# Kernel tuning notes

Hardware: AMD Instinct MI355X
Metric: run time of the kernel (lower is better)

## Reference

```python
import jax, jax.numpy as jnp
import numpy as np

B, S, D, H, L, V = 8, 512, 1024, 16, 12, 30145
FF = 4 * D
NL = 2  # n_langs
EPS = 1e-12


def _ln(x, g, b):
    m = jnp.mean(x, axis=-1, keepdims=True)
    v = jnp.var(x, axis=-1, keepdims=True)
    return (x - m) * jax.lax.rsqrt(v + EPS) * g + b


def setup_inputs() -> dict:
    key = jax.random.key(0)
    ks = iter(jax.random.split(key, 32))
    std, estd = 0.02, 0.02
    d = {
        "input_ids": jax.random.randint(next(ks), (B, S), 0, V),
        "langs": jax.random.randint(next(ks), (B, S), 0, NL),
        "attention_mask": jnp.ones((B, S), jnp.float32),
        "word_emb": jax.random.normal(next(ks), (V, D), jnp.float32) * estd,
        "pos_emb": jax.random.normal(next(ks), (S, D), jnp.float32) * estd,
        "lang_emb": jax.random.normal(next(ks), (NL, D), jnp.float32) * estd,
        "ln_emb_g": jnp.ones((D,), jnp.float32),
        "ln_emb_b": jnp.zeros((D,), jnp.float32),
        "Wq": jax.random.normal(next(ks), (L, D, D), jnp.float32) * std,
        "bq": jnp.zeros((L, D), jnp.float32),
        "Wk": jax.random.normal(next(ks), (L, D, D), jnp.float32) * std,
        "bk": jnp.zeros((L, D), jnp.float32),
        "Wv": jax.random.normal(next(ks), (L, D, D), jnp.float32) * std,
        "bv": jnp.zeros((L, D), jnp.float32),
        "Wo": jax.random.normal(next(ks), (L, D, D), jnp.float32) * std,
        "bo": jnp.zeros((L, D), jnp.float32),
        "ln1_g": jnp.ones((L, D), jnp.float32),
        "ln1_b": jnp.zeros((L, D), jnp.float32),
        "W1": jax.random.normal(next(ks), (L, D, FF), jnp.float32) * std,
        "b1": jnp.zeros((L, FF), jnp.float32),
        "W2": jax.random.normal(next(ks), (L, FF, D), jnp.float32) * std,
        "b2": jnp.zeros((L, D), jnp.float32),
        "ln2_g": jnp.ones((L, D), jnp.float32),
        "ln2_b": jnp.zeros((L, D), jnp.float32),
    }
    return d


def reference(input_ids, langs, attention_mask, word_emb, pos_emb, lang_emb,
              ln_emb_g, ln_emb_b, Wq, bq, Wk, bk, Wv, bv, Wo, bo,
              ln1_g, ln1_b, W1, b1, W2, b2, ln2_g, ln2_b):
    dh = D // H
    scale = 1.0 / np.sqrt(dh).astype(np.float32)
    # embeddings: word + position + language, then LayerNorm, then pad-mask
    x = word_emb[input_ids] + pos_emb[None, :, :] + lang_emb[langs]  # [B,S,D]
    x = _ln(x, ln_emb_g, ln_emb_b)
    fmask = attention_mask  # [B,S], 1=keep
    x = x * fmask[:, :, None]
    neg = (-1e30) * (1.0 - fmask)[:, None, None, :]  # [B,1,1,S] additive mask

    def layer(x, p):
        Wq_, bq_, Wk_, bk_, Wv_, bv_, Wo_, bo_, g1, gb1, W1_, b1_, W2_, b2_, g2, gb2 = p
        q = ((x @ Wq_ + bq_) * scale).reshape(B, S, H, dh)
        k = (x @ Wk_ + bk_).reshape(B, S, H, dh)
        v = (x @ Wv_ + bv_).reshape(B, S, H, dh)
        scores = jnp.einsum('bqhd,bkhd->bhqk', q, k) + neg
        w = jax.nn.softmax(scores, axis=-1)
        ctx = jnp.einsum('bhqk,bkhd->bqhd', w, v).reshape(B, S, D)
        x = _ln(x + ctx @ Wo_ + bo_, g1, gb1)
        h = jax.nn.gelu(x @ W1_ + b1_, approximate=False)  # erf gelu as in source
        x = _ln(x + h @ W2_ + b2_, g2, gb2)
        x = x * fmask[:, :, None]
        return x, None

    params = (Wq, bq, Wk, bk, Wv, bv, Wo, bo, ln1_g, ln1_b, W1, b1, W2, b2, ln2_g, ln2_b)
    x, _ = jax.lax.scan(layer, x, params)
    return x
```

## Files before the change

### kernel.cpp

```cpp
#include <hip/hip_runtime.h>
#include <math.h>

typedef float  f32x4  __attribute__((ext_vector_type(4)));
typedef __bf16 bf16x8 __attribute__((ext_vector_type(8)));
typedef __bf16 bf16x4 __attribute__((ext_vector_type(4)));

#define DEV __device__ __forceinline__

DEV f32x4 mfma16(bf16x8 a, bf16x8 b, f32x4 c) {
    return __builtin_amdgcn_mfma_f32_16x16x32_bf16(a, b, c, 0, 0, 0);
}

DEV void async16(const void* g, void* l) {
    __builtin_amdgcn_global_load_lds((const __attribute__((address_space(1))) void*)g,
                                     (__attribute__((address_space(3))) void*)l, 16, 0, 0);
}

constexpr int B_  = 8;
constexpr int S_  = 512;
constexpr int D_  = 1024;
constexpr int H_  = 16;
constexpr int FF_ = 4096;
constexpr int ROWS = B_ * S_;

__global__ __launch_bounds__(256)
void embed_ln_kernel(const int* __restrict__ ids, const int* __restrict__ lgs,
                     const float* __restrict__ fmask,
                     const float* __restrict__ wemb, const float* __restrict__ pemb,
                     const float* __restrict__ lemb,
                     const float* __restrict__ g, const float* __restrict__ bb,
                     __bf16* __restrict__ xb)
{
    __shared__ float2 red[4];
    const int row = blockIdx.x;
    const int s   = row & (S_ - 1);
    const int t   = threadIdx.x;
    const int lane = t & 63, w = t >> 6;
    const int id = ids[row], lg = lgs[row];

    float4 wv = *(const float4*)(wemb + ((size_t)id << 10) + t * 4);
    float4 pv = *(const float4*)(pemb + ((size_t)s  << 10) + t * 4);
    float4 lv = *(const float4*)(lemb + ((size_t)lg << 10) + t * 4);
    float a[4] = { wv.x + pv.x + lv.x, wv.y + pv.y + lv.y,
                   wv.z + pv.z + lv.z, wv.w + pv.w + lv.w };

    float sm = a[0] + a[1] + a[2] + a[3];
    float sq = a[0]*a[0] + a[1]*a[1] + a[2]*a[2] + a[3]*a[3];
#pragma unroll
    for (int o = 32; o > 0; o >>= 1) { sm += __shfl_down(sm, o); sq += __shfl_down(sq, o); }
    if (lane == 0) red[w] = make_float2(sm, sq);
    __syncthreads();
    float ts = red[0].x + red[1].x + red[2].x + red[3].x;
    float tq = red[0].y + red[1].y + red[2].y + red[3].y;
    float mean = ts * (1.0f / D_);
    float var  = tq * (1.0f / D_) - mean * mean;
    float rs   = rsqrtf(var + 1e-12f);
    float fm   = fmask[row];

    float4 gv = *(const float4*)(g  + t * 4);
    float4 bv = *(const float4*)(bb + t * 4);
    bf16x4 ob;
    ob[0] = (__bf16)(((a[0]-mean)*rs*gv.x + bv.x) * fm);
    ob[1] = (__bf16)(((a[1]-mean)*rs*gv.y + bv.y) * fm);
    ob[2] = (__bf16)(((a[2]-mean)*rs*gv.z + bv.z) * fm);
    ob[3] = (__bf16)(((a[3]-mean)*rs*gv.w + bv.w) * fm);
    *(bf16x4*)(xb + ((size_t)row << 10) + t * 4) = ob;
}

template<int NP>
__global__ __launch_bounds__(128)
void ln_resN_kernel(const __bf16* __restrict__ xres, const __bf16* __restrict__ yp,
                    const float* __restrict__ g, const float* __restrict__ bb,
                    const float* __restrict__ fmask,
                    __bf16* __restrict__ xb_out, float* __restrict__ fout)
{
    constexpr size_t MN = (size_t)ROWS * D_;
    __shared__ float2 red[2];
    const int row = blockIdx.x;
    const int t   = threadIdx.x;
    const int lane = t & 63, w = t >> 6;
    const size_t base = ((size_t)row << 10) + t * 8;

    bf16x8 xv = *(const bf16x8*)(xres + base);
    float a[8];
#pragma unroll
    for (int j = 0; j < 8; ++j) a[j] = (float)xv[j];
#pragma unroll
    for (int pslice = 0; pslice < NP; ++pslice) {
        bf16x8 yv = *(const bf16x8*)(yp + base + (size_t)pslice * MN);
#pragma unroll
        for (int j = 0; j < 8; ++j) a[j] += (float)yv[j];
    }

    float sm = 0.f, sq = 0.f;
#pragma unroll
    for (int j = 0; j < 8; ++j) { sm += a[j]; sq += a[j] * a[j]; }
#pragma unroll
    for (int o = 32; o > 0; o >>= 1) { sm += __shfl_down(sm, o); sq += __shfl_down(sq, o); }
    if (lane == 0) red[w] = make_float2(sm, sq);
    __syncthreads();
    float ts = red[0].x + red[1].x;
    float tq = red[0].y + red[1].y;
    float mean = ts * (1.0f / D_);
    float var  = tq * (1.0f / D_) - mean * mean;
    float rs   = rsqrtf(var + 1e-12f);
    float fm   = fmask ? fmask[row] : 1.0f;

    float4 gv0 = *(const float4*)(g  + t * 8);
    float4 gv1 = *(const float4*)(g  + t * 8 + 4);
    float4 bv0 = *(const float4*)(bb + t * 8);
    float4 bv1 = *(const float4*)(bb + t * 8 + 4);
    float gg[8] = { gv0.x, gv0.y, gv0.z, gv0.w, gv1.x, gv1.y, gv1.z, gv1.w };
    float bbv[8] = { bv0.x, bv0.y, bv0.z, bv0.w, bv1.x, bv1.y, bv1.z, bv1.w };

    float o[8];
    bf16x8 ob;
#pragma unroll
    for (int j = 0; j < 8; ++j) {
        o[j] = ((a[j] - mean) * rs * gg[j] + bbv[j]) * fm;
        ob[j] = (__bf16)o[j];
    }
    *(bf16x8*)(xb_out + base) = ob;
    if (fout) {
        *(float4*)(fout + base)     = make_float4(o[0], o[1], o[2], o[3]);
        *(float4*)(fout + base + 4) = make_float4(o[4], o[5], o[6], o[7]);
    }
}

__global__ __launch_bounds__(256)
void conv_all_kernel(const float* __restrict__ Wq, const float* __restrict__ Wk,
                     const float* __restrict__ Wv, const float* __restrict__ Wo,
                     const float* __restrict__ W1, const float* __restrict__ W2,
                     __bf16* __restrict__ qkvT, __bf16* __restrict__ woT,
                     __bf16* __restrict__ w1T, __bf16* __restrict__ w2T)
{
    __shared__ unsigned int tile32[128 * 130];
    const int id = blockIdx.x;
    const int l  = id / 384;
    int t = id - l * 384;
    const size_t woff = (size_t)l * D_ * D_;
    const size_t foff = (size_t)l * D_ * FF_;
    const float* src; __bf16* dst; int K, N;
    if (t < 128) {
        const int m = t >> 5; t &= 31; K = 1024; N = 1024;
        src = ((m == 0) ? Wq : (m == 1) ? Wk : (m == 2) ? Wv : Wo) + woff;
        dst = (m == 3) ? (woT + woff)
                       : (qkvT + (size_t)l * 3 * D_ * D_ + (size_t)m * D_ * D_);
    } else if (t < 256) {
        t -= 128; K = 1024; N = 4096; src = W1 + foff; dst = w1T + foff;
    } else {
        t -= 256; K = 4096; N = 1024; src = W2 + foff; dst = w2T + foff;
    }
    const int ksup = K >> 8;
    const int tk = t % ksup, tn = t / ksup;
    const int k0s = tk << 8, n0t = tn << 7;
    const int tt = threadIdx.x;

    const int lane32 = tt & 31;
    const int pair   = tt >> 5;
    const int swzr   = (lane32 >> 2) << 2;

#pragma unroll
    for (int it = 0; it < 16; ++it) {
        const int rl = it * 16 + pair * 2;
        const float4 f0 = *(const float4*)(src + (size_t)(k0s + rl)     * N + n0t + lane32 * 4);
        const float4 f1 = *(const float4*)(src + (size_t)(k0s + rl + 1) * N + n0t + lane32 * 4);
        const int j = (rl >> 1) ^ swzr;
        const float lo[4] = { f0.x, f0.y, f0.z, f0.w };
        const float hi[4] = { f1.x, f1.y, f1.z, f1.w };
#pragma unroll
        for (int c = 0; c < 4; ++c) {
            union { unsigned int u; __bf16 b[2]; } pk;
            pk.b[0] = (__bf16)lo[c];
            pk.b[1] = (__bf16)hi[c];
            tile32[(lane32 * 4 + c) * 130 + j] = pk.u;
        }
    }
    __syncthreads();

#pragma unroll
    for (int it = 0; it < 16; ++it) {
        const int n = it * 8 + pair;
        const int jb = (lane32 * 4) ^ ((n >> 4) << 2);
        const unsigned int* tp = tile32 + n * 130 + jb;
        union { unsigned int u[4]; bf16x8 v; } o;
        o.u[0] = tp[0]; o.u[1] = tp[1]; o.u[2] = tp[2]; o.u[3] = tp[3];
        *(bf16x8*)(dst + (size_t)(n0t + n) * K + k0s + lane32 * 8) = o.v;
    }
}

template<int EPI>
__global__ __launch_bounds__(512, 2)
void gemm256_kernel(const __bf16* __restrict__ A, const __bf16* __restrict__ Bt,
                    const float* __restrict__ b0, const float* __restrict__ b1,
                    const float* __restrict__ b2,
                    __bf16* __restrict__ o0, __bf16* __restrict__ o1,
                    __bf16* __restrict__ o2, __bf16* __restrict__ oP,
                    int M, int N, int K, int Kloc, int nTn, int tiles)
{
    __shared__ __bf16 lds[65536];
    const int tid  = threadIdx.x;
    const int lane = tid & 63;
    const int w    = tid >> 6;
    const int wr   = w >> 2, wc = w & 3;

    const int nwg = gridDim.x, bid = blockIdx.x;
    const int cpx = nwg >> 3;
    const int bswz = (bid & 7) * cpx + (bid >> 3);
    const int slice = bswz / tiles;
    const int tile  = bswz % tiles;
    const int bm = tile / nTn, bn = tile % nTn;
    const int m0 = bm << 8, n0 = bn << 8;
    const int ks = slice * Kloc;

    const int rrT = tid >> 3;
    const size_t swzK  = (size_t)(((tid & 7) ^ (rrT & 7)) * 8);
    const size_t aoff0 = (size_t)rrT * K + swzK;
    const size_t boff0 = (size_t)((rrT >> 5) * 64 + (rrT & 31)) * K + swzK;
    const size_t boff1 = (size_t)(((rrT >> 5) + 2) * 64 + (rrT & 31)) * K + swzK;
    const int wub = w * 512;

    const int aread = (wr * 64 + (lane & 15)) * 64;
    const int bread = (wc * 32 + (lane & 15)) * 64;
    const int csw0 = ((      (lane >> 4) * 16) ^ ((lane & 7) << 4)) >> 1;
    const int csw1 = ((64 +  (lane >> 4) * 16) ^ ((lane & 7) << 4)) >> 1;

    f32x4 acc[8][4] = {};
    bf16x8 a_[4][2], b_[2][2];

#define ST_A(p,h,kt) do {                                                     \
    const size_t gb = (size_t)(m0 + (h) * 64) * K + (kt);                     \
    async16(A + gb + aoff0,                  lds + ((p)*2+(h))*8192 + wub);   \
    async16(A + gb + (size_t)128*K + aoff0,  lds + ((p)*2+(h))*8192 + 4096 + wub); \
} while (0)
#define ST_B(p,h,kt) do {                                                     \
    const size_t gb = (size_t)(n0 + (h) * 32) * K + (kt);                     \
    async16(Bt + gb + boff0, lds + 32768 + ((p)*2+(h))*8192 + wub);           \
    async16(Bt + gb + boff1, lds + 32768 + ((p)*2+(h))*8192 + 4096 + wub);    \
} while (0)
#define DS_A(p,h) do {                                                        \
    const __bf16* base_ = lds + ((p)*2+(h))*8192 + aread;                     \
    _Pragma("unroll") for (int m_ = 0; m_ < 4; ++m_) {                        \
        a_[m_][0] = *(const bf16x8*)(base_ + m_*1024 + csw0);                 \
        a_[m_][1] = *(const bf16x8*)(base_ + m_*1024 + csw1);                 \
    }                                                                         \
} while (0)
#define DS_B(p,h) do {                                                        \
    const __bf16* base_ = lds + 32768 + ((p)*2+(h))*8192 + bread;             \
    _Pragma("unroll") for (int n_ = 0; n_ < 2; ++n_) {                        \
        b_[n_][0] = *(const bf16x8*)(base_ + n_*1024 + csw0);                 \
        b_[n_][1] = *(const bf16x8*)(base_ + n_*1024 + csw1);                 \
    }                                                                         \
} while (0)
#define MM(mb,nb) do {                                                        \
    _Pragma("unroll") for (int m_ = 0; m_ < 4; ++m_)                          \
    _Pragma("unroll") for (int n_ = 0; n_ < 2; ++n_)                          \
    _Pragma("unroll") for (int k_ = 0; k_ < 2; ++k_)                          \
        acc[(mb)+m_][(nb)+n_] = mfma16(a_[m_][k_], b_[n_][k_], acc[(mb)+m_][(nb)+n_]); \
} while (0)
#define SYNC do { __builtin_amdgcn_s_barrier();                               \
    asm volatile("s_waitcnt lgkmcnt(0)" ::: "memory");                        \
    __builtin_amdgcn_s_setprio(1); } while (0)
#define PEND do { __builtin_amdgcn_s_setprio(0);                              \
    __builtin_amdgcn_s_barrier(); } while (0)

    ST_A(0,0, ks);      ST_B(0,1, ks);      ST_A(0,1, ks);      ST_B(0,0, ks);
    ST_A(1,0, ks + 64); ST_B(1,1, ks + 64); ST_A(1,1, ks + 64);
    asm volatile("s_waitcnt vmcnt(6)" ::: "memory");
    __builtin_amdgcn_s_barrier();

    const int nIter = Kloc >> 7;
    for (int i = 0; i < nIter; ++i) {
        const bool nl = (i != nIter - 1);
        const int kt1 = ks + (2*i+1) * 64;
        const int kt2 = ks + (2*i+2) * 64;
        const int kt3 = kt2 + 64;
        DS_A(0,0); DS_B(0,0); ST_B(1,0,kt1);
        SYNC; MM(0,0); PEND;
        DS_B(0,1); if (nl) ST_A(0,0,kt2);
        SYNC; MM(0,2); PEND;
        DS_A(0,1); if (nl) ST_B(0,1,kt2);
        SYNC; MM(4,2); PEND;
        DS_B(0,0); if (nl) ST_A(0,1,kt2);
        SYNC; MM(4,0);
        __builtin_amdgcn_s_setprio(0);
        if (nl) asm volatile("s_waitcnt vmcnt(6)" ::: "memory");
        else    asm volatile("s_waitcnt vmcnt(0)" ::: "memory");
        __builtin_amdgcn_s_barrier();
        DS_A(1,0); DS_B(1,0); if (nl) ST_B(0,0,kt2);
        SYNC; MM(0,0); PEND;
        DS_B(1,1); if (nl) ST_A(1,0,kt3);
        SYNC; MM(0,2); PEND;
        DS_A(1,1); if (nl) ST_B(1,1,kt3);
        SYNC; MM(4,2); PEND;
        DS_B(1,0); if (nl) ST_A(1,1,kt3);
        SYNC; MM(4,0);
        __builtin_amdgcn_s_setprio(0);
        if (nl) asm volatile("s_waitcnt vmcnt(6)" ::: "memory");
        __builtin_amdgcn_s_barrier();
    }
#undef ST_A
#undef ST_B
#undef DS_A
#undef DS_B
#undef MM
#undef SYNC
#undef PEND

    const int mrow = m0 + wr * 128 + (lane >> 4) * 4;
    const int ncol = n0 + wc * 64 + (lane & 15);
    if (EPI == 0) {
        const int sel = n0 >> 10;
        const int nc = ncol & 1023;
        if (sel < 2) {
            __bf16* out = (sel == 0) ? o0 : o1;
            const float* bp = (sel == 0) ? b0 : b1;
            const float scl = (sel == 0) ? 0.125f : 1.0f;
#pragma unroll
            for (int ni = 0; ni < 4; ++ni) {
                const float bvv = bp[nc + ni * 16];
#pragma unroll
                for (int mi = 0; mi < 8; ++mi)
#pragma unroll
                    for (int r = 0; r < 4; ++r)
                        out[(size_t)(mrow + mi * 16 + r) * D_ + nc + ni * 16] =
                            (__bf16)((acc[mi][ni][r] + bvv) * scl);
            }
        } else {
#pragma unroll
            for (int ni = 0; ni < 4; ++ni) {
                const int dhf = nc + ni * 16;
                const float bvv = b2[dhf];
                const int hh = dhf >> 6, dh = dhf & 63;
#pragma unroll
                for (int mi = 0; mi < 8; ++mi) {
                    const int gm0 = mrow + mi * 16;
                    const int bb_ = gm0 >> 9, s0 = gm0 & 511;
                    bf16x4 pk;
#pragma unroll
                    for (int r = 0; r < 4; ++r) pk[r] = (__bf16)(acc[mi][ni][r] + bvv);
                    *(bf16x4*)(o2 + ((size_t)((bb_ * 16 + hh) * 64 + dh) << 9) + s0) = pk;
                }
            }
        }
    } else if (EPI == 2) {
#pragma unroll
        for (int ni = 0; ni < 4; ++ni) {
            const float bvv = b0[ncol + ni * 16];
#pragma unroll
            for (int mi = 0; mi < 8; ++mi)
#pragma unroll
                for (int r = 0; r < 4; ++r) {
                    float v = acc[mi][ni][r] + bvv;
                    float u2 = 1.5957691216f * v * (1.0f + 0.044715f * v * v);
                    float ge = v / (1.0f + __expf(-u2));
                    o0[(size_t)(mrow + mi * 16 + r) * N + ncol + ni * 16] = (__bf16)ge;
                }
        }
    } else {
        __bf16* Y = oP + (size_t)slice * M * N;
#pragma unroll
        for (int ni = 0; ni < 4; ++ni) {
            const float bvv = (slice == 0) ? b0[ncol + ni * 16] : 0.0f;
#pragma unroll
            for (int mi = 0; mi < 8; ++mi)
#pragma unroll
                for (int r = 0; r < 4; ++r)
                    Y[(size_t)(mrow + mi * 16 + r) * N + ncol + ni * 16] =
                        (__bf16)(acc[mi][ni][r] + bvv);
        }
    }
}

__global__ __launch_bounds__(256, 2)
void gemm_kernel(const __bf16* __restrict__ A, const __bf16* __restrict__ Bt,
                 const float* __restrict__ bias, __bf16* __restrict__ Cb,
                 int M, int N, int K)
{
    __shared__ __bf16 As[128 * 64];
    __shared__ __bf16 Bs[128 * 64];
    const int tid = threadIdx.x;
    const int lane = tid & 63;
    const int w = tid >> 6, wr = w >> 1, wc = w & 1;
    const int nT = N >> 7;
    const int nwg = gridDim.x;
    const int bid = blockIdx.x;
    const int cpx = nwg >> 3;
    const int bswz = (bid & 7) * cpx + (bid >> 3);
    const int bm = bswz / nT, bn = bswz % nT;
    const int m0 = bm << 7, n0 = bn << 7;

    f32x4 acc[4][4] = {};

    const int chr = tid >> 3, chc = tid & 7;
    const __bf16* ga = A  + (size_t)(m0 + chr) * K + chc * 8;
    const __bf16* gb = Bt + (size_t)(n0 + chr) * K + chc * 8;
    char* la = (char*)As + (tid & ~63) * 16;
    char* lb = (char*)Bs + (tid & ~63) * 16;

    const __bf16* arow = As + (wr * 64 + (lane & 15)) * 64 + (lane >> 4) * 8;
    const __bf16* brow = Bs + (wc * 64 + (lane & 15)) * 64 + (lane >> 4) * 8;

    for (int k0 = 0; k0 < K; k0 += 64) {
#pragma unroll
        for (int i = 0; i < 4; ++i) {
            async16(ga + (size_t)(i * 32) * K + k0, la + i * 4096);
            async16(gb + (size_t)(i * 32) * K + k0, lb + i * 4096);
        }
        __syncthreads();
#pragma unroll
        for (int kk = 0; kk < 2; ++kk) {
            bf16x8 af[4], bf[4];
#pragma unroll
            for (int i = 0; i < 4; ++i) af[i] = *(const bf16x8*)(arow + i * 16 * 64 + kk * 32);
#pragma unroll
            for (int i = 0; i < 4; ++i) bf[i] = *(const bf16x8*)(brow + i * 16 * 64 + kk * 32);
#pragma unroll
            for (int mi = 0; mi < 4; ++mi)
#pragma unroll
                for (int ni = 0; ni < 4; ++ni)
                    acc[mi][ni] = mfma16(af[mi], bf[ni], acc[mi][ni]);
        }
        __syncthreads();
    }

    const int mb = m0 + wr * 64 + ((lane >> 4) * 4);
    const int nb = n0 + wc * 64 + (lane & 15);
#pragma unroll
    for (int ni = 0; ni < 4; ++ni) {
        const float bvv = bias[nb + ni * 16];
#pragma unroll
        for (int mi = 0; mi < 4; ++mi)
#pragma unroll
            for (int r = 0; r < 4; ++r)
                Cb[(size_t)(mb + mi * 16 + r) * N + nb + ni * 16] =
                    (__bf16)(acc[mi][ni][r] + bvv);
    }
}

__global__ __launch_bounds__(512, 1)
void attn_kernel(const __bf16* __restrict__ q, const __bf16* __restrict__ k,
                 const __bf16* __restrict__ vT, const float* __restrict__ fmask,
                 __bf16* __restrict__ ctx)
{
    __shared__ __bf16 Ks[512 * 64];
    __shared__ __bf16 Vt[64 * 512];
    const int bid = blockIdx.x;
    const int qt = bid & 3, h = (bid >> 2) & 15, b = bid >> 6;
    const int tid = threadIdx.x, lane = tid & 63, w = tid >> 6;
    const int g = lane >> 4, q15 = lane & 15, r7 = lane & 7;

    const __bf16* kbase  = k  + ((size_t)b * S_) * D_ + h * 64;
    const __bf16* vTbase = vT + ((size_t)((b * 16 + h) * 64) << 9);
    const float*  fmb    = fmask + b * S_;
    char* kl = (char*)Ks + (tid & ~63) * 16;
    char* vl = (char*)Vt + (tid & ~63) * 16;
    const int srow  = tid >> 3;
    const int sslot = (tid & 7) ^ (srow & 7);

#pragma unroll
    for (int i = 0; i < 8; ++i) {
        const int s = i * 64 + srow;
        async16(kbase + (size_t)s * D_ + sslot * 8, kl + i * 8192);
    }
#pragma unroll
    for (int i = 0; i < 8; ++i) {
        const int d = i * 8 + w;
        async16(vTbase + ((size_t)d << 9) + (((tid & 63) ^ (d & 7)) << 3), vl + i * 8192);
    }

    const __bf16* qbase = q + ((size_t)b * S_ + qt * 128 + w * 16) * D_ + h * 64;
    const bf16x8 qf0 = *(const bf16x8*)(qbase + (size_t)q15 * D_ + g * 8);
    const bf16x8 qf1 = *(const bf16x8*)(qbase + (size_t)q15 * D_ + 32 + g * 8);

    f32x4 sc[32];
#pragma unroll
    for (int i = 0; i < 32; ++i) { sc[i][0] = 0.f; sc[i][1] = 0.f; sc[i][2] = 0.f; sc[i][3] = 0.f; }

    __syncthreads();
#pragma unroll
    for (int nf = 0; nf < 32; ++nf) {
        const __bf16* kr = Ks + (nf * 16 + q15) * 64;
        const bf16x8 kf0 = *(const bf16x8*)(kr + ((g ^ r7) << 3));
        const bf16x8 kf1 = *(const bf16x8*)(kr + (((g + 4) ^ r7) << 3));
        sc[nf] = mfma16(kf0, qf0, sc[nf]);
        sc[nf] = mfma16(kf1, qf1, sc[nf]);
    }

    float mx = -3e38f;
#pragma unroll
    for (int i = 0; i < 32; ++i) {
        const float4 fm4 = *(const float4*)(fmb + i * 16 + 4 * g);
        sc[i][0] += (fm4.x - 1.0f) * 1e30f;
        sc[i][1] += (fm4.y - 1.0f) * 1e30f;
        sc[i][2] += (fm4.z - 1.0f) * 1e30f;
        sc[i][3] += (fm4.w - 1.0f) * 1e30f;
        mx = fmaxf(mx, fmaxf(fmaxf(sc[i][0], sc[i][1]), fmaxf(sc[i][2], sc[i][3])));
    }
    mx = fmaxf(mx, __shfl_xor(mx, 16));
    mx = fmaxf(mx, __shfl_xor(mx, 32));
    float sum = 0.f;
#pragma unroll
    for (int i = 0; i < 32; ++i)
#pragma unroll
        for (int r = 0; r < 4; ++r) { float pp = __expf(sc[i][r] - mx); sc[i][r] = pp; sum += pp; }
    sum += __shfl_xor(sum, 16);
    sum += __shfl_xor(sum, 32);
    const float inv = 1.0f / sum;

    __bf16* P = Ks + w * 4096;
    f32x4 co[4] = {};
#define WR_P(c) do { _Pragma("unroll") for (int i_ = 0; i_ < 16; ++i_) {      \
        bf16x4 pk;                                                            \
        _Pragma("unroll") for (int r = 0; r < 4; ++r) pk[r] = (__bf16)sc[(c)*16+i_][r]; \
        *(bf16x4*)(P + q15 * 256 + ((i_ * 16 + 4 * g) ^ (8 * r7))) = pk; } } while (0)
#define PV(c) do { _Pragma("unroll") for (int kt = 0; kt < 8; ++kt) {         \
        const bf16x8 pf = *(const bf16x8*)(P + q15 * 256 + ((kt * 32 + 8 * g) ^ (8 * r7))); \
        _Pragma("unroll") for (int nf = 0; nf < 4; ++nf) {                    \
            const int d_ = nf * 16 + q15;                                     \
            const bf16x8 vf = *(const bf16x8*)(Vt + d_ * 512 +                \
                (((c) * 256 + kt * 32 + 8 * g) ^ (8 * r7)));                  \
            co[nf] = mfma16(vf, pf, co[nf]); } } } while (0)

    __syncthreads();
    WR_P(0);
    __syncthreads();
    PV(0);
    __syncthreads();
    WR_P(1);
    __syncthreads();
    PV(1);
#undef WR_P
#undef PV

    __bf16* cb = ctx + ((size_t)b * S_ + qt * 128 + w * 16 + q15) * D_ + h * 64;
#pragma unroll
    for (int nf = 0; nf < 4; ++nf) {
        bf16x4 o4;
#pragma unroll
        for (int r = 0; r < 4; ++r) o4[r] = (__bf16)(co[nf][r] * inv);
        *(bf16x4*)(cb + nf * 16 + 4 * g) = o4;
    }
}

extern "C" void kernel_launch(void* const* d_in, const int* in_sizes, int n_in,
                              void* d_out, int out_size, void* d_ws, size_t ws_size,
                              hipStream_t stream)
{
    (void)in_sizes; (void)n_in; (void)out_size; (void)ws_size;
    const int*   ids   = (const int*)d_in[0];
    const int*   lgs   = (const int*)d_in[1];
    const float* amask = (const float*)d_in[2];
    const float* wemb  = (const float*)d_in[3];
    const float* pemb  = (const float*)d_in[4];
    const float* lemb  = (const float*)d_in[5];
    const float* lng   = (const float*)d_in[6];
    const float* lnbv  = (const float*)d_in[7];
    const float* Wq = (const float*)d_in[8];  const float* bq = (const float*)d_in[9];
    const float* Wk = (const float*)d_in[10]; const float* bk = (const float*)d_in[11];
    const float* Wv = (const float*)d_in[12]; const float* bv = (const float*)d_in[13];
    const float* Wo = (const float*)d_in[14]; const float* bo = (const float*)d_in[15];
    const float* g1 = (const float*)d_in[16]; const float* be1 = (const float*)d_in[17];
    const float* W1 = (const float*)d_in[18]; const float* b1 = (const float*)d_in[19];
    const float* W2 = (const float*)d_in[20]; const float* b2 = (const float*)d_in[21];
    const float* g2 = (const float*)d_in[22]; const float* be2 = (const float*)d_in[23];

    char* p = (char*)d_ws;
    auto take = [&](size_t n) { char* r = p; p += (n + 255) & ~(size_t)255; return r; };
    __bf16* xb    = (__bf16*)take((size_t)ROWS * D_ * 2);
    __bf16* qb    = (__bf16*)take((size_t)ROWS * D_ * 2);
    __bf16* kb    = (__bf16*)take((size_t)ROWS * D_ * 2);
    __bf16* vT    = (__bf16*)take((size_t)ROWS * D_ * 2);
    __bf16* cxb   = (__bf16*)take((size_t)ROWS * D_ * 2);
    __bf16* hb    = (__bf16*)take((size_t)ROWS * FF_ * 2);
    __bf16* ybp   = (__bf16*)take((size_t)4 * ROWS * D_ * 2);
    __bf16* wqkvT = (__bf16*)take((size_t)12 * 3 * D_ * D_ * 2);
    __bf16* woT   = (__bf16*)take((size_t)12 * D_ * D_ * 2);
    __bf16* w1T   = (__bf16*)take((size_t)12 * D_ * FF_ * 2);
    __bf16* w2T   = (__bf16*)take((size_t)12 * FF_ * D_ * 2);

    const int gQKV = (ROWS / 256) * (3 * D_ / 256);
    const int gF1  = (ROWS / 256) * (FF_ / 256);
    const int gF2  = 4 * (ROWS / 256) * (D_ / 256);
    const int gWo  = (ROWS / 128) * (D_ / 128);

    conv_all_kernel<<<12 * 384, 256, 0, stream>>>(Wq, Wk, Wv, Wo, W1, W2,
                                                  wqkvT, woT, w1T, w2T);

    embed_ln_kernel<<<ROWS, 256, 0, stream>>>(ids, lgs, amask, wemb, pemb, lemb, lng, lnbv, xb);

    for (int l = 0; l < 12; ++l) {
        __bf16* wqkvL = wqkvT + (size_t)l * 3 * D_ * D_;
        __bf16* woL   = woT   + (size_t)l * D_ * D_;
        __bf16* w1L   = w1T   + (size_t)l * D_ * FF_;
        __bf16* w2L   = w2T   + (size_t)l * FF_ * D_;

        gemm256_kernel<0><<<gQKV, 512, 0, stream>>>(xb, wqkvL, bq + l * D_, bk + l * D_, bv + l * D_,
                                                    qb, kb, vT, nullptr,
                                                    ROWS, 3 * D_, D_, D_, 12, gQKV);

        attn_kernel<<<B_ * H_ * (S_ / 128), 512, 0, stream>>>(qb, kb, vT, amask, cxb);

        gemm_kernel<<<gWo, 256, 0, stream>>>(cxb, woL, bo + l * D_, ybp, ROWS, D_, D_);
        ln_resN_kernel<1><<<ROWS, 128, 0, stream>>>(xb, ybp, g1 + l * D_, be1 + l * D_,
                                                    nullptr, xb, nullptr);

        gemm256_kernel<2><<<gF1, 512, 0, stream>>>(xb, w1L, b1 + l * FF_, nullptr, nullptr,
                                                   hb, nullptr, nullptr, nullptr,
                                                   ROWS, FF_, D_, D_, 16, gF1);
        gemm256_kernel<3><<<gF2, 512, 0, stream>>>(hb, w2L, b2 + l * D_, nullptr, nullptr,
                                                   nullptr, nullptr, nullptr, ybp,
                                                   ROWS, D_, FF_, D_, 4, 64);

        float* dst = (l == 11) ? (float*)d_out : nullptr;
        ln_resN_kernel<4><<<ROWS, 128, 0, stream>>>(xb, ybp, g2 + l * D_, be2 + l * D_,
                                                    amask, xb, dst);
    }
}
```

Baseline: 2.468 ms.

## Fuse residual LayerNorm into GEMM epilogues using per-row-tile atomic completion counters

Removes the two standalone residual+LayerNorm kernels per layer. Each GEMM block now bumps an atomic counter for its row tile, and the last block to finish that tile applies residual-add, LayerNorm, masking and the optional fp32 output for all its rows. This saves kernel launches and a separate pass over the activations. In exchange, each tile's LayerNorm runs inside a single block, which can create a serialized tail, and correctness depends on threadfence ordering and counters that are reset by a memset on every call.

```diff
diff --git a/kernel.cpp b/kernel.cpp
--- a/kernel.cpp
+++ b/kernel.cpp
@@ -22,6 +22,56 @@
 constexpr int H_  = 16;
 constexpr int FF_ = 4096;
 constexpr int ROWS = B_ * S_;
+
+DEV void ln_row(int row, __bf16* xio, const __bf16* yp, int NP,
+                const float* g, const float* bb, const float* fmask,
+                float* fout, int l64)
+{
+    const size_t MN = (size_t)ROWS * D_;
+    const size_t rb = ((size_t)row << 10) + l64 * 16;
+    float a[16];
+    bf16x8 x0 = *(const bf16x8*)(xio + rb);
+    bf16x8 x1 = *(const bf16x8*)(xio + rb + 8);
+#pragma unroll
+    for (int j = 0; j < 8; ++j) { a[j] = (float)x0[j]; a[8 + j] = (float)x1[j]; }
+    for (int s = 0; s < NP; ++s) {
+        bf16x8 y0 = *(const bf16x8*)(yp + rb + (size_t)s * MN);
+        bf16x8 y1 = *(const bf16x8*)(yp + rb + (size_t)s * MN + 8);
+#pragma unroll
+        for (int j = 0; j < 8; ++j) { a[j] += (float)y0[j]; a[8 + j] += (float)y1[j]; }
+    }
+    float sm = 0.f, sq = 0.f;
+#pragma unroll
+    for (int j = 0; j < 16; ++j) { sm += a[j]; sq += a[j] * a[j]; }
+#pragma unroll
+    for (int o = 32; o > 0; o >>= 1) { sm += __shfl_xor(sm, o); sq += __shfl_xor(sq, o); }
+    const float mean = sm * (1.0f / D_);
+    const float var  = sq * (1.0f / D_) - mean * mean;
+    const float rs   = rsqrtf(var + 1e-12f);
+    const float fm   = fmask ? fmask[row] : 1.0f;
+    float ov[16];
+#pragma unroll
+    for (int q = 0; q < 4; ++q) {
+        float4 gv = *(const float4*)(g  + l64 * 16 + q * 4);
+        float4 bv = *(const float4*)(bb + l64 * 16 + q * 4);
+        const float gq[4] = { gv.x, gv.y, gv.z, gv.w };
+        const float bq[4] = { bv.x, bv.y, bv.z, bv.w };
+#pragma unroll
+        for (int j = 0; j < 4; ++j)
+            ov[q * 4 + j] = ((a[q * 4 + j] - mean) * rs * gq[j] + bq[j]) * fm;
+    }
+    bf16x8 ob0, ob1;
+#pragma unroll
+    for (int j = 0; j < 8; ++j) { ob0[j] = (__bf16)ov[j]; ob1[j] = (__bf16)ov[8 + j]; }
+    *(bf16x8*)(xio + rb)     = ob0;
+    *(bf16x8*)(xio + rb + 8) = ob1;
+    if (fout) {
+#pragma unroll
+        for (int q = 0; q < 4; ++q)
+            *(float4*)(fout + rb + q * 4) =
+                make_float4(ov[q*4], ov[q*4+1], ov[q*4+2], ov[q*4+3]);
+    }
+}
 
 __global__ __launch_bounds__(256)
 void embed_ln_kernel(const int* __restrict__ ids, const int* __restrict__ lgs,
@@ -65,66 +115,6 @@
     ob[2] = (__bf16)(((a[2]-mean)*rs*gv.z + bv.z) * fm);
     ob[3] = (__bf16)(((a[3]-mean)*rs*gv.w + bv.w) * fm);
     *(bf16x4*)(xb + ((size_t)row << 10) + t * 4) = ob;
-}
-
-template<int NP>
-__global__ __launch_bounds__(128)
-void ln_resN_kernel(const __bf16* __restrict__ xres, const __bf16* __restrict__ yp,
-                    const float* __restrict__ g, const float* __restrict__ bb,
-                    const float* __restrict__ fmask,
-                    __bf16* __restrict__ xb_out, float* __restrict__ fout)
-{
-    constexpr size_t MN = (size_t)ROWS * D_;
-    __shared__ float2 red[2];
-    const int row = blockIdx.x;
-    const int t   = threadIdx.x;
-    const int lane = t & 63, w = t >> 6;
-    const size_t base = ((size_t)row << 10) + t * 8;
-
-    bf16x8 xv = *(const bf16x8*)(xres + base);
-    float a[8];
-#pragma unroll
-    for (int j = 0; j < 8; ++j) a[j] = (float)xv[j];
-#pragma unroll
-    for (int pslice = 0; pslice < NP; ++pslice) {
-        bf16x8 yv = *(const bf16x8*)(yp + base + (size_t)pslice * MN);
-#pragma unroll
-        for (int j = 0; j < 8; ++j) a[j] += (float)yv[j];
-    }
-
-    float sm = 0.f, sq = 0.f;
-#pragma unroll
-    for (int j = 0; j < 8; ++j) { sm += a[j]; sq += a[j] * a[j]; }
-#pragma unroll
-    for (int o = 32; o > 0; o >>= 1) { sm += __shfl_down(sm, o); sq += __shfl_down(sq, o); }
-    if (lane == 0) red[w] = make_float2(sm, sq);
-    __syncthreads();
-    float ts = red[0].x + red[1].x;
-    float tq = red[0].y + red[1].y;
-    float mean = ts * (1.0f / D_);
-    float var  = tq * (1.0f / D_) - mean * mean;
-    float rs   = rsqrtf(var + 1e-12f);
-    float fm   = fmask ? fmask[row] : 1.0f;
-
-    float4 gv0 = *(const float4*)(g  + t * 8);
-    float4 gv1 = *(const float4*)(g  + t * 8 + 4);
-    float4 bv0 = *(const float4*)(bb + t * 8);
-    float4 bv1 = *(const float4*)(bb + t * 8 + 4);
-    float gg[8] = { gv0.x, gv0.y, gv0.z, gv0.w, gv1.x, gv1.y, gv1.z, gv1.w };
-    float bbv[8] = { bv0.x, bv0.y, bv0.z, bv0.w, bv1.x, bv1.y, bv1.z, bv1.w };
-
-    float o[8];
-    bf16x8 ob;
-#pragma unroll
-    for (int j = 0; j < 8; ++j) {
-        o[j] = ((a[j] - mean) * rs * gg[j] + bbv[j]) * fm;
-        ob[j] = (__bf16)o[j];
-    }
-    *(bf16x8*)(xb_out + base) = ob;
-    if (fout) {
-        *(float4*)(fout + base)     = make_float4(o[0], o[1], o[2], o[3]);
-        *(float4*)(fout + base + 4) = make_float4(o[4], o[5], o[6], o[7]);
-    }
 }
 
 __global__ __launch_bounds__(256)
@@ -196,9 +186,12 @@
                     const float* __restrict__ b2,
                     __bf16* __restrict__ o0, __bf16* __restrict__ o1,
                     __bf16* __restrict__ o2, __bf16* __restrict__ oP,
-                    int M, int N, int K, int Kloc, int nTn, int tiles)
+                    int M, int N, int K, int Kloc, int nTn, int tiles,
+                    __bf16* xio, const float* gamma, const float* beta,
+                    const float* fmaskp, float* fout, unsigned int* cnt)
 {
     __shared__ __bf16 lds[65536];
+    __shared__ unsigned int lnflag;
     const int tid  = threadIdx.x;
     const int lane = tid & 63;
     const int w    = tid >> 6;
@@ -370,15 +363,30 @@
                         (__bf16)(acc[mi][ni][r] + bvv);
         }
     }
+
+    if (EPI == 3) {
+        __threadfence();
+        if (tid == 0) lnflag = ((atomicAdd(cnt + bm, 1u) & 15) == 15) ? 1u : 0u;
+        __syncthreads();
+        if (lnflag) {
+            __threadfence();
+            const int wv = tid >> 6, l64 = tid & 63;
+            for (int rr = wv; rr < 256; rr += 8)
+                ln_row(bm * 256 + rr, xio, oP, 4, gamma, beta, fmaskp, fout, l64);
+        }
+    }
 }
 
 __global__ __launch_bounds__(256, 2)
 void gemm_kernel(const __bf16* __restrict__ A, const __bf16* __restrict__ Bt,
                  const float* __restrict__ bias, __bf16* __restrict__ Cb,
-                 int M, int N, int K)
+                 int M, int N, int K,
+                 __bf16* xio, const float* gamma, const float* beta,
+                 unsigned int* cnt)
 {
     __shared__ __bf16 As[128 * 64];
     __shared__ __bf16 Bs[128 * 64];
+    __shared__ unsigned int lnflag;
     const int tid = threadIdx.x;
     const int lane = tid & 63;
     const int w = tid >> 6, wr = w >> 1, wc = w & 1;
@@ -435,6 +443,16 @@
             for (int r = 0; r < 4; ++r)
                 Cb[(size_t)(mb + mi * 16 + r) * N + nb + ni * 16] =
                     (__bf16)(acc[mi][ni][r] + bvv);
+    }
+
+    __threadfence();
+    if (tid == 0) lnflag = ((atomicAdd(cnt + bm, 1u) & 7) == 7) ? 1u : 0u;
+    __syncthreads();
+    if (lnflag) {
+        __threadfence();
+        const int wv = tid >> 6, l64 = tid & 63;
+        for (int rr = wv; rr < 128; rr += 4)
+            ln_row(bm * 128 + rr, xio, Cb, 1, gamma, beta, nullptr, nullptr, l64);
     }
 }
 
@@ -578,11 +596,14 @@
     __bf16* woT   = (__bf16*)take((size_t)12 * D_ * D_ * 2);
     __bf16* w1T   = (__bf16*)take((size_t)12 * D_ * FF_ * 2);
     __bf16* w2T   = (__bf16*)take((size_t)12 * FF_ * D_ * 2);
+    unsigned int* cnt = (unsigned int*)take(12 * 64 * 4);
 
     const int gQKV = (ROWS / 256) * (3 * D_ / 256);
     const int gF1  = (ROWS / 256) * (FF_ / 256);
     const int gF2  = 4 * (ROWS / 256) * (D_ / 256);
     const int gWo  = (ROWS / 128) * (D_ / 128);
+
+    hipMemsetAsync(cnt, 0, 12 * 64 * 4, stream);
 
     conv_all_kernel<<<12 * 384, 256, 0, stream>>>(Wq, Wk, Wv, Wo, W1, W2,
                                                   wqkvT, woT, w1T, w2T);
@@ -594,26 +615,28 @@
         __bf16* woL   = woT   + (size_t)l * D_ * D_;
         __bf16* w1L   = w1T   + (size_t)l * D_ * FF_;
         __bf16* w2L   = w2T   + (size_t)l * FF_ * D_;
+        unsigned int* cntL = cnt + l * 64;
 
         gemm256_kernel<0><<<gQKV, 512, 0, stream>>>(xb, wqkvL, bq + l * D_, bk + l * D_, bv + l * D_,
                                                     qb, kb, vT, nullptr,
-                                                    ROWS, 3 * D_, D_, D_, 12, gQKV);
+                                                    ROWS, 3 * D_, D_, D_, 12, gQKV,
+                                                    nullptr, nullptr, nullptr, nullptr, nullptr, nullptr);
 
         attn_kernel<<<B_ * H_ * (S_ / 128), 512, 0, stream>>>(qb, kb, vT, amask, cxb);
 
-        gemm_kernel<<<gWo, 256, 0, stream>>>(cxb, woL, bo + l * D_, ybp, ROWS, D_, D_);
-        ln_resN_kernel<1><<<ROWS, 128, 0, stream>>>(xb, ybp, g1 + l * D_, be1 + l * D_,
-                                                    nullptr, xb, nullptr);
+        gemm_kernel<<<gWo, 256, 0, stream>>>(cxb, woL, bo + l * D_, ybp, ROWS, D_, D_,
+                                             xb, g1 + l * D_, be1 + l * D_, cntL);
 
         gemm256_kernel<2><<<gF1, 512, 0, stream>>>(xb, w1L, b1 + l * FF_, nullptr, nullptr,
                                                    hb, nullptr, nullptr, nullptr,
-                                                   ROWS, FF_, D_, D_, 16, gF1);
+                                                   ROWS, FF_, D_, D_, 16, gF1,
+                                                   nullptr, nullptr, nullptr, nullptr, nullptr, nullptr);
+
         gemm256_kernel<3><<<gF2, 512, 0, stream>>>(hb, w2L, b2 + l * D_, nullptr, nullptr,
                                                    nullptr, nullptr, nullptr, ybp,
-                                                   ROWS, D_, FF_, D_, 4, 64);
-
-        float* dst = (l == 11) ? (float*)d_out : nullptr;
-        ln_resN_kernel<4><<<ROWS, 128, 0, stream>>>(xb, ybp, g2 + l * D_, be2 + l * D_,
-                                                    amask, xb, dst);
-    }
-}
+                                                   ROWS, D_, FF_, D_, 4, 64,
+                                                   xb, g2 + l * D_, be2 + l * D_, amask,
+                                                   (l == 11) ? (float*)d_out : nullptr,
+                                                   cntL + 32);
+    }
+}
```

After: 4.754 ms. 92.6% more time.
